# Kernel tuning notes

Hardware: AMD Instinct MI355X
Metric: run time of the kernel (lower is better)

Reference implementation:

```python
import jax, jax.numpy as jnp
import numpy as np

B, S, HID = 2, 2048, 1024
NH, HD = 16, 64  # op_heads, head_size; op_size = NH*HD = 1024


def setup_inputs() -> dict:
    key = jax.random.key(0)
    k1, k2, k3 = jax.random.split(key, 3)
    hidden_states = jax.random.normal(k1, (B, S, HID), dtype=jnp.float32)
    # Linear weights stored as [in, out] for x @ W + b
    Wqk = jax.random.normal(k2, (HID, 2 * NH * HD), dtype=jnp.float32) * (HID ** -0.5)
    bqk = jnp.zeros((2 * NH * HD,), dtype=jnp.float32)
    Wv = jax.random.normal(k3, (HID, NH * HD), dtype=jnp.float32) * (HID ** -0.5)
    bv = jnp.zeros((NH * HD,), dtype=jnp.float32)
    return {"hidden_states": hidden_states, "Wqk": Wqk, "bqk": bqk, "Wv": Wv, "bv": bv}


def _split_heads(t):
    # [B, S, NH*HD] -> [B, NH, S, HD]
    b, s, _ = t.shape
    return t.reshape(b, s, NH, HD).transpose(0, 2, 1, 3)


def reference(hidden_states, Wqk, bqk, Wv, bv):
    op_size = NH * HD
    qk = hidden_states @ Wqk + bqk                      # [B, S, 2*op_size]
    query, key = qk[..., :op_size], qk[..., op_size:]
    value = hidden_states @ Wv + bv                     # [B, S, op_size]
    q = _split_heads(query)                             # [B, H, S, D]
    k = _split_heads(key)
    v = _split_heads(value)
    # scores: [B, H, Sq, Sk], scaled by sqrt(head_dim) (scale_attn_weights=True)
    scores = jnp.einsum('bhqd,bhkd->bhqk', q, k) / jnp.asarray(HD ** 0.5, q.dtype)
    s = scores.shape[-1]
    causal = jnp.tril(jnp.ones((s, s), dtype=bool))     # [S, S]
    mask_value = jnp.finfo(scores.dtype).min
    scores = jnp.where(causal, scores, mask_value)
    attn = jax.nn.softmax(scores, axis=-1)              # dropout is identity (eval)
    out = jnp.einsum('bhqk,bhkd->bhqd', attn, v)        # [B, H, S, D]
    out = out.transpose(0, 2, 1, 3).reshape(out.shape[0], out.shape[2], NH * HD)
    return out
```

## Files before the change

### kernel.cpp

```cpp
#include <hip/hip_runtime.h>

typedef float floatx4 __attribute__((ext_vector_type(4)));
typedef float floatx16 __attribute__((ext_vector_type(16)));
typedef __bf16 bf16x8 __attribute__((ext_vector_type(8)));
typedef unsigned short u16x8 __attribute__((ext_vector_type(8)));
typedef unsigned short u16x4 __attribute__((ext_vector_type(4)));

#define GLDS16(g, l) __builtin_amdgcn_global_load_lds( \
    (__attribute__((address_space(1))) void*)(g), \
    (__attribute__((address_space(3))) void*)(l), 16, 0, 0)

__device__ __forceinline__ unsigned short f2bf(float f) {
    unsigned u = __float_as_uint(f);
    u += 0x7fffu + ((u >> 16) & 1u);
    return (unsigned short)(u >> 16);
}

#if __has_builtin(__builtin_amdgcn_cvt_pk_bf16_f32)
__device__ __forceinline__ unsigned pk2(float a, float b) {
    typedef __bf16 bf16x2 __attribute__((ext_vector_type(2)));
    union { bf16x2 v; unsigned u; } cv;
    cv.v = __builtin_amdgcn_cvt_pk_bf16_f32(a, b);
    return cv.u;
}
#else
__device__ __forceinline__ unsigned pk2(float a, float b) {
    return (unsigned)f2bf(a) | ((unsigned)f2bf(b) << 16);
}
#endif

#if __has_builtin(__builtin_amdgcn_exp2f)
__device__ __forceinline__ float fast_exp2(float x) { return __builtin_amdgcn_exp2f(x); }
#else
__device__ __forceinline__ float fast_exp2(float x) { return __exp2f(x); }
#endif

__global__ __launch_bounds__(256) void k_convert(const float* __restrict__ in,
                                                 unsigned short* __restrict__ out) {
    int idx = (blockIdx.x * 256 + threadIdx.x) * 8;
    const float4* p = (const float4*)(in + idx);
    float4 f0 = p[0], f1 = p[1];
    u16x8 o;
    o[0] = f2bf(f0.x); o[1] = f2bf(f0.y); o[2] = f2bf(f0.z); o[3] = f2bf(f0.w);
    o[4] = f2bf(f1.x); o[5] = f2bf(f1.y); o[6] = f2bf(f1.z); o[7] = f2bf(f1.w);
    *(u16x8*)(out + idx) = o;
}

__global__ __launch_bounds__(256) void k_transpose(const float* __restrict__ Wqk,
                                                   const float* __restrict__ Wv,
                                                   unsigned short* __restrict__ Wt) {
    __shared__ unsigned short t[64][68];
    const int tid = threadIdx.x;
    const int n0 = blockIdx.x * 64;
    const int k0 = blockIdx.y * 64;
    const int nl = tid & 63;
    const int kb = tid >> 6;
    const int ng = n0 + nl;
#pragma unroll
    for (int i = 0; i < 16; ++i) {
        int kl = kb + i * 4;
        float v = (n0 < 2048) ? Wqk[(size_t)(k0 + kl) * 2048 + ng]
                              : Wv[(size_t)(k0 + kl) * 1024 + (ng - 2048)];
        t[nl][kl] = f2bf(v);
    }
    __syncthreads();
    const int k4 = (tid & 15) * 4;
    const int nb = tid >> 4;
#pragma unroll
    for (int i = 0; i < 4; ++i) {
        int n2 = nb + i * 16;
        u16x4 o;
        o[0] = t[n2][k4]; o[1] = t[n2][k4 + 1]; o[2] = t[n2][k4 + 2]; o[3] = t[n2][k4 + 3];
        *(u16x4*)(Wt + (size_t)(n0 + n2) * 1024 + k0 + k4) = o;
    }
}

__global__ __launch_bounds__(256, 2) void k_gemm_qkv(
    const unsigned short* __restrict__ A,
    const unsigned short* __restrict__ Bt,
    const float* __restrict__ bqk, const float* __restrict__ bvv,
    unsigned short* __restrict__ Qf, unsigned short* __restrict__ Kf,
    unsigned short* __restrict__ Vf) {
    __shared__ unsigned short As[128 * 32];
    __shared__ unsigned short Bs[128 * 32];
    const int tid = threadIdx.x;
    const int lane = tid & 63;
    const int w = tid >> 6;
    const int l15 = lane & 15;
    const int quad = lane >> 4;
    const int m0 = blockIdx.x * 128;
    const int n0 = blockIdx.y * 128;
    const int wm = (w & 1) * 64;
    const int wn = (w >> 1) * 64;
    const int rC = lane >> 2;
    const int kC = (lane & 3) * 8;
    const int c0 = w * 2;

    floatx4 acc[4][4] = {};

    const unsigned short* agp0 = A + (size_t)(m0 + c0 * 16 + rC) * 1024 + kC;
    const unsigned short* agp1 = agp0 + 16 * 1024;
    const unsigned short* bgp0 = Bt + (size_t)(n0 + c0 * 16 + rC) * 1024 + kC;
    const unsigned short* bgp1 = bgp0 + 16 * 1024;
    unsigned short* al = As + c0 * 512;
    unsigned short* bl = Bs + c0 * 512;

    for (int k0 = 0; k0 < 1024; k0 += 32) {
        GLDS16(agp0 + k0, al);
        GLDS16(agp1 + k0, al + 512);
        GLDS16(bgp0 + k0, bl);
        GLDS16(bgp1 + k0, bl + 512);
        __syncthreads();
        const unsigned short* ap = As + (wm + l15) * 32 + quad * 8;
        const unsigned short* bp = Bs + (wn + l15) * 32 + quad * 8;
        bf16x8 af[4], bfr[4];
#pragma unroll
        for (int mi = 0; mi < 4; ++mi) af[mi] = *(const bf16x8*)(ap + mi * 16 * 32);
#pragma unroll
        for (int ni = 0; ni < 4; ++ni) bfr[ni] = *(const bf16x8*)(bp + ni * 16 * 32);
#pragma unroll
        for (int mi = 0; mi < 4; ++mi)
#pragma unroll
            for (int ni = 0; ni < 4; ++ni)
                acc[mi][ni] = __builtin_amdgcn_mfma_f32_16x16x32_bf16(af[mi], bfr[ni],
                                                                      acc[mi][ni], 0, 0, 0);
        __syncthreads();
    }
#pragma unroll
    for (int ni = 0; ni < 4; ++ni) {
        const int n = n0 + wn + ni * 16 + l15;
        if (n < 2048) {
            const float bias = bqk[n];
            const bool isQ = n < 1024;
            unsigned short* dst = isQ ? Qf : Kf;
            const int hd = isQ ? n : n - 1024;
            const float scale = isQ ? 0.18033688011112042f : 1.0f;
            const int h = hd >> 6, d = hd & 63;
            const int kb = d >> 4, hhd = (d >> 3) & 1, jj = d & 7;
#pragma unroll
            for (int mi = 0; mi < 4; ++mi)
#pragma unroll
                for (int r = 0; r < 4; ++r) {
                    const int m = m0 + wm + mi * 16 + (quad << 2) + r;
                    const int b = m >> 11, s = m & 2047;
                    const int bh = b * 16 + h, t = s >> 5, cc = s & 31;
                    size_t idx = ((((size_t)(bh * 64 + t) * 4 + kb) * 2 + hhd) * 32 + cc) * 8 + jj;
                    dst[idx] = f2bf((acc[mi][ni][r] + bias) * scale);
                }
        } else {
            const float bias = bvv[n - 2048];
            const int hd = n - 2048;
            const int h = hd >> 6, d = hd & 63;
            const int dt = d >> 5, cc = d & 31;
#pragma unroll
            for (int mi = 0; mi < 4; ++mi) {
                const int m = m0 + wm + mi * 16 + (quad << 2);
                const int b = m >> 11, s = m & 2047;
                const int bh = b * 16 + h, t = s >> 5, kvr = s & 31;
                const int mb = kvr >> 4, hhv = (kvr >> 3) & 1, jj0 = s & 7;
                u16x4 o4;
#pragma unroll
                for (int r = 0; r < 4; ++r) o4[r] = f2bf(acc[mi][ni][r] + bias);
                size_t idx = (((((size_t)(bh * 64 + t) * 2 + mb) * 2 + dt) * 2 + hhv) * 32 + cc) * 8 + jj0;
                *(u16x4*)(Vf + idx) = o4;
            }
        }
    }
}

__global__ __launch_bounds__(64, 3) void k_attn(
    const unsigned short* __restrict__ Qf, const unsigned short* __restrict__ Kf,
    const unsigned short* __restrict__ Vf, float* __restrict__ out,
    float* __restrict__ Op1, float* __restrict__ l0, float* __restrict__ l1) {
    const int lane = threadIdx.x;
    const int c = lane & 31;
    const int hh = lane >> 5;
    const int gb = blockIdx.x;
    const int bh = ((gb & 7) << 2) | ((gb >> 3) & 3);
    const int u = gb >> 5;
    int j, t0, t1, mode;
    if (u < 32) { j = 63 - u; t0 = 0; t1 = 31; mode = 1; }
    else {
        const int uu = u - 32, i = uu >> 1;
        if ((uu & 1) == 0) { j = 63 - i; t0 = 32; t1 = j; mode = 2; }
        else               { j = 31 - i; t0 = 0;  t1 = j; mode = 0; }
    }
    const int q_abs = j * 32 + c;

    bf16x8 qf[4];
    {
        const unsigned short* qp = Qf + (size_t)(bh * 64 + j) * 2048 + lane * 8;
#pragma unroll
        for (int kb = 0; kb < 4; ++kb) qf[kb] = *(const bf16x8*)(qp + kb * 512);
    }
    const unsigned short* kbase = Kf + (size_t)bh * (64 * 2048) + lane * 8;
    const unsigned short* vbase = Vf + (size_t)bh * (64 * 2048) + lane * 8;

    floatx16 o2[2] = {};
    float ls0 = 0.f, ls1 = 0.f;

    bf16x8 kf[4];
    {
        const unsigned short* kp = kbase + (size_t)t0 * 2048;
#pragma unroll
        for (int kb = 0; kb < 4; ++kb) kf[kb] = *(const bf16x8*)(kp + kb * 512);
    }

    for (int t = t0; t <= t1; ++t) {
        const unsigned short* vp = vbase + (size_t)t * 2048;
        bf16x8 vf[4];
#pragma unroll
        for (int f = 0; f < 4; ++f) vf[f] = *(const bf16x8*)(vp + f * 512);

        floatx16 st = {};
#pragma unroll
        for (int kb = 0; kb < 4; ++kb)
            st = __builtin_amdgcn_mfma_f32_32x32x16_bf16(kf[kb], qf[kb], st, 0, 0, 0);

        bf16x8 kn[4];
        if (t < t1) {
            const unsigned short* kpn = kbase + (size_t)(t + 1) * 2048;
#pragma unroll
            for (int kb = 0; kb < 4; ++kb) kn[kb] = *(const bf16x8*)(kpn + kb * 512);
        }

        if (t == j) {
#pragma unroll
            for (int i = 0; i < 16; ++i) {
                const int kvr = (i & 3) + 8 * (i >> 2) + 4 * hh;
                if (kvr > c) st[i] = -1e30f;
            }
        }

        float a0 = 0.f, a1 = 0.f, a2 = 0.f, a3 = 0.f;
#pragma unroll
        for (int i = 0; i < 16; i += 4) {
            float p0 = fast_exp2(st[i + 0]);
            float p1 = fast_exp2(st[i + 1]);
            float p2 = fast_exp2(st[i + 2]);
            float p3 = fast_exp2(st[i + 3]);
            st[i + 0] = p0; st[i + 1] = p1; st[i + 2] = p2; st[i + 3] = p3;
            a0 += p0; a1 += p1; a2 += p2; a3 += p3;
        }
        ls0 += a0 + a2; ls1 += a1 + a3;

#pragma unroll
        for (int mb = 0; mb < 2; ++mb) {
            const int rb = mb * 8;
            unsigned p0 = pk2(st[rb + 0], st[rb + 1]);
            unsigned p1 = pk2(st[rb + 2], st[rb + 3]);
            unsigned p2 = pk2(st[rb + 4], st[rb + 5]);
            unsigned p3 = pk2(st[rb + 6], st[rb + 7]);
            unsigned sA = hh ? p0 : p2;
            unsigned sB = hh ? p1 : p3;
            unsigned rA = (unsigned)__shfl_xor((int)sA, 32, 64);
            unsigned rB = (unsigned)__shfl_xor((int)sB, 32, 64);
            union { unsigned u4[4]; bf16x8 v; } pf;
            if (hh == 0) { pf.u4[0] = p0; pf.u4[1] = p1; pf.u4[2] = rA; pf.u4[3] = rB; }
            else         { pf.u4[0] = rA; pf.u4[1] = rB; pf.u4[2] = p2; pf.u4[3] = p3; }
#pragma unroll
            for (int dt = 0; dt < 2; ++dt)
                o2[dt] = __builtin_amdgcn_mfma_f32_32x32x16_bf16(vf[mb * 2 + dt], pf.v,
                                                                 o2[dt], 0, 0, 0);
        }
#pragma unroll
        for (int kb = 0; kb < 4; ++kb) kf[kb] = kn[kb];
    }

    const int b = bh >> 4, head = bh & 15;
    float lrow = ls0 + ls1;
    lrow += __shfl_xor(lrow, 32, 64);
    if (mode == 0) {
        const float inv = 1.0f / lrow;
        float* op = out + (size_t)(b * 2048 + q_abs) * 1024 + head * 64;
#pragma unroll
        for (int dt = 0; dt < 2; ++dt)
#pragma unroll
            for (int rr = 0; rr < 4; ++rr) {
                float4 v4 = make_float4(o2[dt][rr * 4 + 0] * inv, o2[dt][rr * 4 + 1] * inv,
                                        o2[dt][rr * 4 + 2] * inv, o2[dt][rr * 4 + 3] * inv);
                *(float4*)(op + dt * 32 + rr * 8 + hh * 4) = v4;
            }
    } else {
        const int qr = q_abs - 1024;
        float* op;
        if (mode == 1) {
            if (hh == 0) l0[bh * 1024 + qr] = lrow;
            op = out + (size_t)(b * 2048 + q_abs) * 1024 + head * 64;
        } else {
            if (hh == 0) l1[bh * 1024 + qr] = lrow;
            op = Op1 + (size_t)(bh * 1024 + qr) * 64;
        }
#pragma unroll
        for (int dt = 0; dt < 2; ++dt)
#pragma unroll
            for (int rr = 0; rr < 4; ++rr) {
                float4 v4 = make_float4(o2[dt][rr * 4 + 0], o2[dt][rr * 4 + 1],
                                        o2[dt][rr * 4 + 2], o2[dt][rr * 4 + 3]);
                *(float4*)(op + dt * 32 + rr * 8 + hh * 4) = v4;
            }
    }
}

__global__ __launch_bounds__(256) void k_comb(const float* __restrict__ Op1,
                                              const float* __restrict__ l0,
                                              const float* __restrict__ l1,
                                              float* __restrict__ out) {
    const int idx = blockIdx.x * 256 + threadIdx.x;
    const int bh = idx >> 14;
    const int rem = idx & 16383;
    const int qr = rem >> 4;
    const int d4 = (rem & 15) << 2;
    const float inv = 1.0f / (l0[bh * 1024 + qr] + l1[bh * 1024 + qr]);
    const int b = bh >> 4, h = bh & 15;
    float* op = out + (size_t)(b * 2048 + 1024 + qr) * 1024 + h * 64 + d4;
    const float* pp = Op1 + (size_t)(bh * 1024 + qr) * 64 + d4;
    float4 a = *(const float4*)op;
    float4 p = *(const float4*)pp;
    float4 r = make_float4((a.x + p.x) * inv, (a.y + p.y) * inv,
                           (a.z + p.z) * inv, (a.w + p.w) * inv);
    *(float4*)op = r;
}

extern "C" void kernel_launch(void* const* d_in, const int* in_sizes, int n_in,
                              void* d_out, int out_size, void* d_ws, size_t ws_size,
                              hipStream_t stream) {
    const float* hidden = (const float*)d_in[0];
    const float* Wqk    = (const float*)d_in[1];
    const float* bqk    = (const float*)d_in[2];
    const float* Wv     = (const float*)d_in[3];
    const float* bvv    = (const float*)d_in[4];
    float* out = (float*)d_out;

    unsigned short* Abf = (unsigned short*)d_ws;
    unsigned short* Wt  = Abf + 4096 * 1024;
    unsigned short* Qf  = Wt + 3072 * 1024;
    unsigned short* Kf  = Qf + 32 * 2048 * 64;
    unsigned short* Vf  = Kf + 32 * 2048 * 64;
    float* Op1 = (float*)d_ws;
    float* l0  = Op1 + 32 * 1024 * 64;
    float* l1  = l0 + 32 * 1024;

    k_convert<<<2048, 256, 0, stream>>>(hidden, Abf);
    k_transpose<<<dim3(48, 16), 256, 0, stream>>>(Wqk, Wv, Wt);
    k_gemm_qkv<<<dim3(32, 24), 256, 0, stream>>>(Abf, Wt, bqk, bvv, Qf, Kf, Vf);
    k_attn<<<3072, 64, 0, stream>>>(Qf, Kf, Vf, out, Op1, l0, l1);
    k_comb<<<2048, 256, 0, stream>>>(Op1, l0, l1, out);
}
```

Measured before the change: 156.1 us.

## Merge convert/transpose kernels and deepen GEMM K-step to 64

```diff
diff --git a/kernel.cpp b/kernel.cpp
--- a/kernel.cpp
+++ b/kernel.cpp
@@ -35,24 +35,26 @@
 __device__ __forceinline__ float fast_exp2(float x) { return __exp2f(x); }
 #endif
 
-__global__ __launch_bounds__(256) void k_convert(const float* __restrict__ in,
-                                                 unsigned short* __restrict__ out) {
-    int idx = (blockIdx.x * 256 + threadIdx.x) * 8;
-    const float4* p = (const float4*)(in + idx);
-    float4 f0 = p[0], f1 = p[1];
-    u16x8 o;
-    o[0] = f2bf(f0.x); o[1] = f2bf(f0.y); o[2] = f2bf(f0.z); o[3] = f2bf(f0.w);
-    o[4] = f2bf(f1.x); o[5] = f2bf(f1.y); o[6] = f2bf(f1.z); o[7] = f2bf(f1.w);
-    *(u16x8*)(out + idx) = o;
-}
-
-__global__ __launch_bounds__(256) void k_transpose(const float* __restrict__ Wqk,
-                                                   const float* __restrict__ Wv,
-                                                   unsigned short* __restrict__ Wt) {
+__global__ __launch_bounds__(256) void k_prep(const float* __restrict__ hidden,
+                                              const float* __restrict__ Wqk,
+                                              const float* __restrict__ Wv,
+                                              unsigned short* __restrict__ Abf,
+                                              unsigned short* __restrict__ Wt) {
     __shared__ unsigned short t[64][68];
     const int tid = threadIdx.x;
-    const int n0 = blockIdx.x * 64;
-    const int k0 = blockIdx.y * 64;
+    if (blockIdx.x < 2048) {
+        int idx = (blockIdx.x * 256 + tid) * 8;
+        const float4* p = (const float4*)(hidden + idx);
+        float4 f0 = p[0], f1 = p[1];
+        u16x8 o;
+        o[0] = f2bf(f0.x); o[1] = f2bf(f0.y); o[2] = f2bf(f0.z); o[3] = f2bf(f0.w);
+        o[4] = f2bf(f1.x); o[5] = f2bf(f1.y); o[6] = f2bf(f1.z); o[7] = f2bf(f1.w);
+        *(u16x8*)(Abf + idx) = o;
+        return;
+    }
+    const int bx = blockIdx.x - 2048;
+    const int n0 = (bx % 48) * 64;
+    const int k0 = (bx / 48) * 64;
     const int nl = tid & 63;
     const int kb = tid >> 6;
     const int ng = n0 + nl;
@@ -75,14 +77,14 @@
     }
 }
 
-__global__ __launch_bounds__(256, 2) void k_gemm_qkv(
+__global__ __launch_bounds__(256, 3) void k_gemm_qkv(
     const unsigned short* __restrict__ A,
     const unsigned short* __restrict__ Bt,
     const float* __restrict__ bqk, const float* __restrict__ bvv,
     unsigned short* __restrict__ Qf, unsigned short* __restrict__ Kf,
     unsigned short* __restrict__ Vf) {
-    __shared__ unsigned short As[128 * 32];
-    __shared__ unsigned short Bs[128 * 32];
+    __shared__ unsigned short As[2][128 * 32];
+    __shared__ unsigned short Bs[2][128 * 32];
     const int tid = threadIdx.x;
     const int lane = tid & 63;
     const int w = tid >> 6;
@@ -102,28 +104,32 @@
     const unsigned short* agp1 = agp0 + 16 * 1024;
     const unsigned short* bgp0 = Bt + (size_t)(n0 + c0 * 16 + rC) * 1024 + kC;
     const unsigned short* bgp1 = bgp0 + 16 * 1024;
-    unsigned short* al = As + c0 * 512;
-    unsigned short* bl = Bs + c0 * 512;
-
-    for (int k0 = 0; k0 < 1024; k0 += 32) {
-        GLDS16(agp0 + k0, al);
-        GLDS16(agp1 + k0, al + 512);
-        GLDS16(bgp0 + k0, bl);
-        GLDS16(bgp1 + k0, bl + 512);
+
+    for (int k0 = 0; k0 < 1024; k0 += 64) {
+#pragma unroll
+        for (int h = 0; h < 2; ++h) {
+            GLDS16(agp0 + k0 + h * 32, &As[h][c0 * 512]);
+            GLDS16(agp1 + k0 + h * 32, &As[h][c0 * 512 + 512]);
+            GLDS16(bgp0 + k0 + h * 32, &Bs[h][c0 * 512]);
+            GLDS16(bgp1 + k0 + h * 32, &Bs[h][c0 * 512 + 512]);
+        }
         __syncthreads();
-        const unsigned short* ap = As + (wm + l15) * 32 + quad * 8;
-        const unsigned short* bp = Bs + (wn + l15) * 32 + quad * 8;
-        bf16x8 af[4], bfr[4];
-#pragma unroll
-        for (int mi = 0; mi < 4; ++mi) af[mi] = *(const bf16x8*)(ap + mi * 16 * 32);
-#pragma unroll
-        for (int ni = 0; ni < 4; ++ni) bfr[ni] = *(const bf16x8*)(bp + ni * 16 * 32);
-#pragma unroll
-        for (int mi = 0; mi < 4; ++mi)
-#pragma unroll
-            for (int ni = 0; ni < 4; ++ni)
-                acc[mi][ni] = __builtin_amdgcn_mfma_f32_16x16x32_bf16(af[mi], bfr[ni],
-                                                                      acc[mi][ni], 0, 0, 0);
+#pragma unroll
+        for (int h = 0; h < 2; ++h) {
+            const unsigned short* ap = &As[h][(wm + l15) * 32 + quad * 8];
+            const unsigned short* bp = &Bs[h][(wn + l15) * 32 + quad * 8];
+            bf16x8 af[4], bfr[4];
+#pragma unroll
+            for (int mi = 0; mi < 4; ++mi) af[mi] = *(const bf16x8*)(ap + mi * 16 * 32);
+#pragma unroll
+            for (int ni = 0; ni < 4; ++ni) bfr[ni] = *(const bf16x8*)(bp + ni * 16 * 32);
+#pragma unroll
+            for (int mi = 0; mi < 4; ++mi)
+#pragma unroll
+                for (int ni = 0; ni < 4; ++ni)
+                    acc[mi][ni] = __builtin_amdgcn_mfma_f32_16x16x32_bf16(af[mi], bfr[ni],
+                                                                          acc[mi][ni], 0, 0, 0);
+        }
         __syncthreads();
     }
 #pragma unroll
@@ -341,8 +347,7 @@
     float* l0  = Op1 + 32 * 1024 * 64;
     float* l1  = l0 + 32 * 1024;
 
-    k_convert<<<2048, 256, 0, stream>>>(hidden, Abf);
-    k_transpose<<<dim3(48, 16), 256, 0, stream>>>(Wqk, Wv, Wt);
+    k_prep<<<2816, 256, 0, stream>>>(hidden, Wqk, Wv, Abf, Wt);
     k_gemm_qkv<<<dim3(32, 24), 256, 0, stream>>>(Abf, Wt, bqk, bvv, Qf, Kf, Vf);
     k_attn<<<3072, 64, 0, stream>>>(Qf, Kf, Vf, out, Op1, l0, l1);
     k_comb<<<2048, 256, 0, stream>>>(Op1, l0, l1, out);
```

New measurement: 156.6 us. No clear change (+0.3%).
